# Kernel optimization log

Measured on AMD Instinct MI355X. Metric: run time of the kernel, lower is better.

## Reference

```python
import jax, jax.numpy as jnp
import numpy as np

TABLE_SIZE = 524288  # 2**19
NUM_LEVELS = 16
F_PER_LEVEL = 2
BASE_RES = 16
MAX_RES = 512
BB_MIN, BB_MAX = -1.0, 1.0
N_POINTS = 524288

_b = np.exp(np.log(MAX_RES / BASE_RES) / (NUM_LEVELS - 1))
RESOLUTIONS = np.array([int(np.floor(BASE_RES * _b ** l)) for l in range(NUM_LEVELS)], dtype=np.float32)
PRIMES = np.array([1, 2654435761, 805459861], dtype=np.uint32)
# 8 cube corners (same order as torch source)
OFFSETS = np.array([[0,0,0],[1,0,0],[0,1,0],[0,0,1],[1,1,0],[1,0,1],[0,1,1],[1,1,1]], dtype=np.float32)


def setup_inputs() -> dict:
    key = jax.random.key(0)
    k1, k2 = jax.random.split(key)
    x = jax.random.uniform(k1, (N_POINTS, 3), jnp.float32, -1.0, 1.0)
    tables = jax.random.normal(k2, (NUM_LEVELS, TABLE_SIZE, F_PER_LEVEL), jnp.float32) * 0.01
    return {"x": x, "tables": tables}


def reference(x, tables):
    # normalize to [0,1) using bounding box
    xn = jnp.clip((x - BB_MIN) / (BB_MAX - BB_MIN), 0.0, 1.0 - 1e-6)
    res = jnp.asarray(RESOLUTIONS)                       # [L]
    xs = xn[None] * res[:, None, None]                   # [L,N,3]
    xf = jnp.floor(xs)
    wf = xs - xf                                         # [L,N,3] trilinear fracs
    off = jnp.asarray(OFFSETS)                           # [8,3]
    # integer corner coords; uint32 wrap preserves hash mod 2**19 (power-of-two table)
    corner = xf[:, :, None, :].astype(jnp.uint32) + off[None, None].astype(jnp.uint32)  # [L,N,8,3]
    primes = jnp.asarray(PRIMES)
    h = (corner[..., 0] * primes[0]) ^ (corner[..., 1] * primes[1]) ^ (corner[..., 2] * primes[2])
    idx = (h % jnp.uint32(TABLE_SIZE)).astype(jnp.int32)  # [L,N,8]
    # trilinear weights: prod over xyz of (1-o)*(1-w) + o*w
    w = jnp.prod((1.0 - off)[None, None] * (1.0 - wf[:, :, None, :])
                 + off[None, None] * wf[:, :, None, :], axis=-1)  # [L,N,8]
    # per-level hashed gather: [L,N,8,F]
    feats = jax.vmap(lambda t, i: t[i])(tables, idx)
    interp = jnp.einsum('lnc,lncf->lnf', w, feats)       # [L,N,F]
    n = x.shape[0]
    return jnp.transpose(interp, (1, 0, 2)).reshape(n, NUM_LEVELS * F_PER_LEVEL)
```

## Files before the change

### kernel.cpp

```cpp
#include <hip/hip_runtime.h>
#include <cstdint>
#include <cstring>

namespace {
constexpr uint32_t kTableSize = 524288u;
constexpr uint32_t kTableMask = kTableSize - 1u;
constexpr uint32_t kP1 = 2654435761u;
constexpr uint32_t kP2 = 805459861u;
}

__constant__ float c_res[16] = {16.f, 20.f, 25.f, 32.f, 40.f, 50.f, 64.f, 80.f,
                                101.f, 128.f, 161.f, 203.f, 256.f, 322.f, 406.f, 512.f};

__device__ __forceinline__ double hash_interp(const float2* __restrict__ tbl,
                                              float px, float py, float pz,
                                              float res)
{
    const float nx = fminf(fmaxf((px + 1.0f) * 0.5f, 0.0f), 0.999999f);
    const float ny = fminf(fmaxf((py + 1.0f) * 0.5f, 0.0f), 0.999999f);
    const float nz = fminf(fmaxf((pz + 1.0f) * 0.5f, 0.0f), 0.999999f);

    const float sx = nx * res, sy = ny * res, sz = nz * res;
    const float fx = floorf(sx), fy = floorf(sy), fz = floorf(sz);
    const float wx = sx - fx, wy = sy - fy, wz = sz - fz;
    const float ixw = 1.0f - wx, iyw = 1.0f - wy, izw = 1.0f - wz;

    const uint32_t cx = (uint32_t)fx;
    const uint32_t cy = (uint32_t)fy;
    const uint32_t cz = (uint32_t)fz;

    const uint32_t hy0 = cy * kP1;    const uint32_t hy1 = hy0 + kP1;
    const uint32_t hz0 = cz * kP2;    const uint32_t hz1 = hz0 + kP2;

    const uint32_t b00 = cx ^ hy0 ^ hz0;
    const uint32_t b10 = cx ^ hy1 ^ hz0;
    const uint32_t b01 = cx ^ hy0 ^ hz1;
    const uint32_t b11 = cx ^ hy1 ^ hz1;

    float2 g0, g1, g2, g3, g4, g5, g6, g7;

    if ((cx & 1u) == 0u) {
        const float* tf = reinterpret_cast<const float*>(tbl);
        {
            const uint32_t ia = b00 & kTableMask;
            const float4 q = *reinterpret_cast<const float4*>(tf + (ia & ~1u) * 2u);
            const bool hi = (ia & 1u);
            g0 = hi ? make_float2(q.z, q.w) : make_float2(q.x, q.y);
            g1 = hi ? make_float2(q.x, q.y) : make_float2(q.z, q.w);
        }
        {
            const uint32_t ia = b10 & kTableMask;
            const float4 q = *reinterpret_cast<const float4*>(tf + (ia & ~1u) * 2u);
            const bool hi = (ia & 1u);
            g2 = hi ? make_float2(q.z, q.w) : make_float2(q.x, q.y);
            g4 = hi ? make_float2(q.x, q.y) : make_float2(q.z, q.w);
        }
        {
            const uint32_t ia = b01 & kTableMask;
            const float4 q = *reinterpret_cast<const float4*>(tf + (ia & ~1u) * 2u);
            const bool hi = (ia & 1u);
            g3 = hi ? make_float2(q.z, q.w) : make_float2(q.x, q.y);
            g5 = hi ? make_float2(q.x, q.y) : make_float2(q.z, q.w);
        }
        {
            const uint32_t ia = b11 & kTableMask;
            const float4 q = *reinterpret_cast<const float4*>(tf + (ia & ~1u) * 2u);
            const bool hi = (ia & 1u);
            g6 = hi ? make_float2(q.z, q.w) : make_float2(q.x, q.y);
            g7 = hi ? make_float2(q.x, q.y) : make_float2(q.z, q.w);
        }
    } else {
        const uint32_t cx1 = cx + 1u;
        g0 = tbl[(b00) & kTableMask];
        g1 = tbl[(cx1 ^ hy0 ^ hz0) & kTableMask];
        g2 = tbl[(b10) & kTableMask];
        g4 = tbl[(cx1 ^ hy1 ^ hz0) & kTableMask];
        g3 = tbl[(b01) & kTableMask];
        g5 = tbl[(cx1 ^ hy0 ^ hz1) & kTableMask];
        g6 = tbl[(b11) & kTableMask];
        g7 = tbl[(cx1 ^ hy1 ^ hz1) & kTableMask];
    }

    const float w0 = (ixw * iyw) * izw;
    const float w1 = (wx  * iyw) * izw;
    const float w2 = (ixw * wy ) * izw;
    const float w3 = (ixw * iyw) * wz;
    const float w4 = (wx  * wy ) * izw;
    const float w5 = (wx  * iyw) * wz;
    const float w6 = (ixw * wy ) * wz;
    const float w7 = (wx  * wy ) * wz;

    float a0 = w0 * g0.x;           float a1 = w0 * g0.y;
    a0 = fmaf(w1, g1.x, a0);        a1 = fmaf(w1, g1.y, a1);
    a0 = fmaf(w2, g2.x, a0);        a1 = fmaf(w2, g2.y, a1);
    a0 = fmaf(w3, g3.x, a0);        a1 = fmaf(w3, g3.y, a1);
    a0 = fmaf(w4, g4.x, a0);        a1 = fmaf(w4, g4.y, a1);
    a0 = fmaf(w5, g5.x, a0);        a1 = fmaf(w5, g5.y, a1);
    a0 = fmaf(w6, g6.x, a0);        a1 = fmaf(w6, g6.y, a1);
    a0 = fmaf(w7, g7.x, a0);        a1 = fmaf(w7, g7.y, a1);

    float2 r = make_float2(a0, a1);
    double rd;
    memcpy(&rd, &r, sizeof(rd));
    return rd;
}

__global__ __launch_bounds__(256) void fine_kernel(
    const float* __restrict__ x,
    const float* __restrict__ tables,
    double* __restrict__ ws,
    int n_points)
{
    const uint32_t xcd = blockIdx.x & 7u;
    const uint32_t j   = blockIdx.x >> 3;
    const uint32_t l   = 8u + xcd;
    const uint32_t p   = j * 256u + threadIdx.x;
    if (p >= (uint32_t)n_points) return;

    const float px = __builtin_nontemporal_load(x + p * 3u + 0u);
    const float py = __builtin_nontemporal_load(x + p * 3u + 1u);
    const float pz = __builtin_nontemporal_load(x + p * 3u + 2u);

    const float2* __restrict__ tbl =
        reinterpret_cast<const float2*>(tables) + (size_t)l * kTableSize;

    const double rd = hash_interp(tbl, px, py, pz, c_res[l]);
    __builtin_nontemporal_store(rd, ws + (size_t)xcd * (uint32_t)n_points + p);
}

__global__ __launch_bounds__(256) void coarse_kernel(
    const float* __restrict__ x,
    const float* __restrict__ tables,
    double* __restrict__ ws,
    int n_points, int n_half)
{
    const uint32_t s = blockIdx.x & 15u;
    const uint32_t j = blockIdx.x >> 4;
    const uint32_t l    = (s < 8u) ? s : (15u - s);
    const uint32_t base = (s < 8u) ? 0u : (uint32_t)n_half;
    const uint32_t lim  = (s < 8u) ? (uint32_t)n_half : (uint32_t)n_points;
    const uint32_t p = base + j * 256u + threadIdx.x;
    if (p >= lim) return;

    const float px = __builtin_nontemporal_load(x + p * 3u + 0u);
    const float py = __builtin_nontemporal_load(x + p * 3u + 1u);
    const float pz = __builtin_nontemporal_load(x + p * 3u + 2u);

    const float2* __restrict__ tbl =
        reinterpret_cast<const float2*>(tables) + (size_t)l * kTableSize;

    const double rd = hash_interp(tbl, px, py, pz, c_res[l]);
    __builtin_nontemporal_store(rd, ws + (size_t)l * (uint32_t)n_points + p);
}

__global__ __launch_bounds__(256) void merge_kernel(
    const double* __restrict__ ws,
    double* __restrict__ out,
    int n_points, int slot_base)
{
    __shared__ double tile[32][9];
    const uint32_t t  = threadIdx.x;
    const uint32_t p0 = blockIdx.x * 32u;

    {
        const uint32_t lvl = t >> 5;
        const uint32_t pi  = t & 31u;
        const uint32_t p   = p0 + pi;
        double v = 0.0;
        if (p < (uint32_t)n_points)
            v = __builtin_nontemporal_load(ws + (size_t)lvl * (uint32_t)n_points + p);
        tile[pi][lvl] = v;
    }
    __syncthreads();
    {
        const uint32_t lvl = t & 7u;
        const uint32_t pi  = t >> 3;
        const uint32_t p   = p0 + pi;
        if (p < (uint32_t)n_points)
            __builtin_nontemporal_store(tile[pi][lvl],
                                        out + (size_t)p * 16u + (uint32_t)slot_base + lvl);
    }
}

__global__ __launch_bounds__(256) void hashenc_fallback(
    const float* __restrict__ x,
    const float* __restrict__ tables,
    float* __restrict__ out,
    int n_points)
{
    const uint32_t tid = blockIdx.x * 256u + threadIdx.x;
    const uint32_t p = tid >> 4;
    const uint32_t l = tid & 15u;
    if (p >= (uint32_t)n_points) return;

    const float px = x[p * 3u + 0u];
    const float py = x[p * 3u + 1u];
    const float pz = x[p * 3u + 2u];

    const float2* __restrict__ tbl =
        reinterpret_cast<const float2*>(tables) + (size_t)l * kTableSize;
    const double rd = hash_interp(tbl, px, py, pz, c_res[l]);
    __builtin_nontemporal_store(rd, reinterpret_cast<double*>(out) + (size_t)p * 16u + l);
}

extern "C" void kernel_launch(void* const* d_in, const int* in_sizes, int n_in,
                              void* d_out, int out_size, void* d_ws, size_t ws_size,
                              hipStream_t stream) {
    const float* x      = (const float*)d_in[0];
    const float* tables = (const float*)d_in[1];
    float* out          = (float*)d_out;

    const int n_points = in_sizes[0] / 3;
    const size_t ws_needed = (size_t)8 * (size_t)n_points * sizeof(double);

    if (ws_size < ws_needed) {
        const int total = n_points * 16;
        const int grid = (total + 255) / 256;
        hashenc_fallback<<<grid, 256, 0, stream>>>(x, tables, out, n_points);
        return;
    }

    double* ws = (double*)d_ws;
    const int n_half = (n_points + 1) / 2;
    const int merge_grid = (n_points + 31) / 32;

    {
        const int chunks = (n_points + 255) / 256;
        fine_kernel<<<chunks * 8, 256, 0, stream>>>(x, tables, ws, n_points);
    }
    merge_kernel<<<merge_grid, 256, 0, stream>>>(ws, (double*)out, n_points, 8);

    {
        const int chunks = (n_half + 255) / 256;
        coarse_kernel<<<chunks * 16, 256, 0, stream>>>(x, tables, ws, n_points, n_half);
    }
    merge_kernel<<<merge_grid, 256, 0, stream>>>(ws, (double*)out, n_points, 0);
}
```

Baseline: 305.5 us.

## Use 16-level workspace with single full-row merge and rebalanced coarse split

When the workspace is large enough, all 16 levels are written to a 16-row workspace and a single merge kernel emits each output row with 16-byte vector stores, replacing two half-merges. The coarse levels are split into two kernels: levels 6 and 7 are quartered across eight block slots, and levels 0-5 are interleaved over 24 slots, to balance the gather load. The aim is to drop one merge pass and its partial-row strided writes, in exchange for double the workspace and one extra launch. The old 8-row path is kept as a fallback.

Result: faster. 296.9 us (-2.8%).

```diff
diff --git a/kernel.cpp b/kernel.cpp
--- a/kernel.cpp
+++ b/kernel.cpp
@@ -8,6 +8,8 @@
 constexpr uint32_t kP1 = 2654435761u;
 constexpr uint32_t kP2 = 805459861u;
 }
+
+typedef double v2d __attribute__((ext_vector_type(2)));
 
 __constant__ float c_res[16] = {16.f, 20.f, 25.f, 32.f, 40.f, 50.f, 64.f, 80.f,
                                 101.f, 128.f, 161.f, 203.f, 256.f, 322.f, 406.f, 512.f};
@@ -105,10 +107,18 @@
     return rd;
 }
 
+__device__ __forceinline__ void load_xyz(const float* __restrict__ x, uint32_t p,
+                                         float& px, float& py, float& pz)
+{
+    px = __builtin_nontemporal_load(x + p * 3u + 0u);
+    py = __builtin_nontemporal_load(x + p * 3u + 1u);
+    pz = __builtin_nontemporal_load(x + p * 3u + 2u);
+}
+
 __global__ __launch_bounds__(256) void fine_kernel(
     const float* __restrict__ x,
     const float* __restrict__ tables,
-    double* __restrict__ ws,
+    double* __restrict__ wsrow,
     int n_points)
 {
     const uint32_t xcd = blockIdx.x & 7u;
@@ -117,18 +127,101 @@
     const uint32_t p   = j * 256u + threadIdx.x;
     if (p >= (uint32_t)n_points) return;
 
-    const float px = __builtin_nontemporal_load(x + p * 3u + 0u);
-    const float py = __builtin_nontemporal_load(x + p * 3u + 1u);
-    const float pz = __builtin_nontemporal_load(x + p * 3u + 2u);
-
-    const float2* __restrict__ tbl =
-        reinterpret_cast<const float2*>(tables) + (size_t)l * kTableSize;
-
-    const double rd = hash_interp(tbl, px, py, pz, c_res[l]);
-    __builtin_nontemporal_store(rd, ws + (size_t)xcd * (uint32_t)n_points + p);
-}
-
-__global__ __launch_bounds__(256) void coarse_kernel(
+    float px, py, pz;
+    load_xyz(x, p, px, py, pz);
+
+    const float2* __restrict__ tbl =
+        reinterpret_cast<const float2*>(tables) + (size_t)l * kTableSize;
+
+    const double rd = hash_interp(tbl, px, py, pz, c_res[l]);
+    __builtin_nontemporal_store(rd, wsrow + (size_t)xcd * (uint32_t)n_points + p);
+}
+
+__global__ __launch_bounds__(256) void coarse_big_kernel(
+    const float* __restrict__ x,
+    const float* __restrict__ tables,
+    double* __restrict__ ws,
+    int n_points, int n_quarter)
+{
+    const uint32_t s = blockIdx.x & 7u;
+    const uint32_t j = blockIdx.x >> 3;
+    const uint32_t l = (s < 4u) ? 7u : 6u;
+    const uint32_t q = s & 3u;
+    const uint32_t base = q * (uint32_t)n_quarter;
+    const uint32_t lim  = min(base + (uint32_t)n_quarter, (uint32_t)n_points);
+    const uint32_t p = base + j * 256u + threadIdx.x;
+    if (p >= lim) return;
+
+    float px, py, pz;
+    load_xyz(x, p, px, py, pz);
+
+    const float2* __restrict__ tbl =
+        reinterpret_cast<const float2*>(tables) + (size_t)l * kTableSize;
+
+    const double rd = hash_interp(tbl, px, py, pz, c_res[l]);
+    __builtin_nontemporal_store(rd, ws + (size_t)l * (uint32_t)n_points + p);
+}
+
+__global__ __launch_bounds__(256) void coarse_small_kernel(
+    const float* __restrict__ x,
+    const float* __restrict__ tables,
+    double* __restrict__ ws,
+    int n_points, int n_quarter)
+{
+    const uint32_t s = blockIdx.x % 24u;
+    const uint32_t j = blockIdx.x / 24u;
+    const uint32_t l = s >> 2;
+    const uint32_t q = s & 3u;
+    const uint32_t base = q * (uint32_t)n_quarter;
+    const uint32_t lim  = min(base + (uint32_t)n_quarter, (uint32_t)n_points);
+    const uint32_t p = base + j * 256u + threadIdx.x;
+    if (p >= lim) return;
+
+    float px, py, pz;
+    load_xyz(x, p, px, py, pz);
+
+    const float2* __restrict__ tbl =
+        reinterpret_cast<const float2*>(tables) + (size_t)l * kTableSize;
+
+    const double rd = hash_interp(tbl, px, py, pz, c_res[l]);
+    __builtin_nontemporal_store(rd, ws + (size_t)l * (uint32_t)n_points + p);
+}
+
+__global__ __launch_bounds__(256) void merge_full_kernel(
+    const double* __restrict__ ws,
+    double* __restrict__ out,
+    int n_points)
+{
+    __shared__ double tile[32][17];
+    const uint32_t t  = threadIdx.x;
+    const uint32_t p0 = blockIdx.x * 32u;
+
+    #pragma unroll
+    for (uint32_t r = 0; r < 2; ++r) {
+        const uint32_t lvl = r * 8u + (t >> 5);
+        const uint32_t pi  = t & 31u;
+        const uint32_t p   = p0 + pi;
+        double v = 0.0;
+        if (p < (uint32_t)n_points)
+            v = __builtin_nontemporal_load(ws + (size_t)lvl * (uint32_t)n_points + p);
+        tile[pi][lvl] = v;
+    }
+    __syncthreads();
+    {
+        const uint32_t pi = t >> 3;
+        const uint32_t j  = t & 7u;
+        const uint32_t p  = p0 + pi;
+        if (p < (uint32_t)n_points) {
+            v2d v;
+            v.x = tile[pi][2u * j + 0u];
+            v.y = tile[pi][2u * j + 1u];
+            __builtin_nontemporal_store(
+                v, reinterpret_cast<v2d*>(out + (size_t)p * 16u) + j);
+        }
+    }
+}
+
+__global__ __launch_bounds__(256) void coarse_kernel_r4(
     const float* __restrict__ x,
     const float* __restrict__ tables,
     double* __restrict__ ws,
@@ -142,9 +235,8 @@
     const uint32_t p = base + j * 256u + threadIdx.x;
     if (p >= lim) return;
 
-    const float px = __builtin_nontemporal_load(x + p * 3u + 0u);
-    const float py = __builtin_nontemporal_load(x + p * 3u + 1u);
-    const float pz = __builtin_nontemporal_load(x + p * 3u + 2u);
+    float px, py, pz;
+    load_xyz(x, p, px, py, pz);
 
     const float2* __restrict__ tbl =
         reinterpret_cast<const float2*>(tables) + (size_t)l * kTableSize;
@@ -153,7 +245,7 @@
     __builtin_nontemporal_store(rd, ws + (size_t)l * (uint32_t)n_points + p);
 }
 
-__global__ __launch_bounds__(256) void merge_kernel(
+__global__ __launch_bounds__(256) void merge_half_kernel(
     const double* __restrict__ ws,
     double* __restrict__ out,
     int n_points, int slot_base)
@@ -161,7 +253,6 @@
     __shared__ double tile[32][9];
     const uint32_t t  = threadIdx.x;
     const uint32_t p0 = blockIdx.x * 32u;
-
     {
         const uint32_t lvl = t >> 5;
         const uint32_t pi  = t & 31u;
@@ -211,28 +302,40 @@
     float* out          = (float*)d_out;
 
     const int n_points = in_sizes[0] / 3;
-    const size_t ws_needed = (size_t)8 * (size_t)n_points * sizeof(double);
-
-    if (ws_size < ws_needed) {
+    const size_t ws16 = (size_t)16 * (size_t)n_points * sizeof(double);
+    const size_t ws8  = (size_t)8  * (size_t)n_points * sizeof(double);
+
+    double* ws = (double*)d_ws;
+
+    if (ws_size >= ws16) {
+        const int n_quarter = (n_points + 3) / 4;
+        const int chunks_n  = (n_points + 255) / 256;
+        const int chunks_q  = (n_quarter + 255) / 256;
+
+        fine_kernel<<<chunks_n * 8, 256, 0, stream>>>(
+            x, tables, ws + (size_t)8 * (uint32_t)n_points, n_points);
+        coarse_big_kernel<<<chunks_q * 8, 256, 0, stream>>>(
+            x, tables, ws, n_points, n_quarter);
+        coarse_small_kernel<<<chunks_q * 24, 256, 0, stream>>>(
+            x, tables, ws, n_points, n_quarter);
+        merge_full_kernel<<<(n_points + 31) / 32, 256, 0, stream>>>(
+            ws, (double*)out, n_points);
+    } else if (ws_size >= ws8) {
+        const int n_half = (n_points + 1) / 2;
+        const int merge_grid = (n_points + 31) / 32;
+        {
+            const int chunks = (n_points + 255) / 256;
+            fine_kernel<<<chunks * 8, 256, 0, stream>>>(x, tables, ws, n_points);
+        }
+        merge_half_kernel<<<merge_grid, 256, 0, stream>>>(ws, (double*)out, n_points, 8);
+        {
+            const int chunks = (n_half + 255) / 256;
+            coarse_kernel_r4<<<chunks * 16, 256, 0, stream>>>(x, tables, ws, n_points, n_half);
+        }
+        merge_half_kernel<<<merge_grid, 256, 0, stream>>>(ws, (double*)out, n_points, 0);
+    } else {
         const int total = n_points * 16;
         const int grid = (total + 255) / 256;
         hashenc_fallback<<<grid, 256, 0, stream>>>(x, tables, out, n_points);
-        return;
-    }
-
-    double* ws = (double*)d_ws;
-    const int n_half = (n_points + 1) / 2;
-    const int merge_grid = (n_points + 31) / 32;
-
-    {
-        const int chunks = (n_points + 255) / 256;
-        fine_kernel<<<chunks * 8, 256, 0, stream>>>(x, tables, ws, n_points);
-    }
-    merge_kernel<<<merge_grid, 256, 0, stream>>>(ws, (double*)out, n_points, 8);
-
-    {
-        const int chunks = (n_half + 255) / 256;
-        coarse_kernel<<<chunks * 16, 256, 0, stream>>>(x, tables, ws, n_points, n_half);
-    }
-    merge_kernel<<<merge_grid, 256, 0, stream>>>(ws, (double*)out, n_points, 0);
-}
+    }
+}
```
